# Kernel tuning notes

Measured on AMD Instinct MI355X. Metric: run time of the kernel, lower is better.

The kernel has to match this reference:

```python
import jax, jax.numpy as jnp
import numpy as np

B, T, D, H = 512, 200, 128, 128


def setup_inputs() -> dict:
    key = jax.random.key(0)
    ks = jax.random.split(key, 16)
    r = lambda k, shp, s=0.05: jax.random.normal(k, shp, dtype=jnp.float32) * s
    F = 3 * D + H  # concat([item_eb, his_sum, item_eb*his_sum, final_state2])
    return {
        "item_eb": jax.random.normal(ks[0], (B, D), dtype=jnp.float32),
        "item_his_eb": jax.random.normal(ks[1], (B, T, D), dtype=jnp.float32),
        "Wg1": r(ks[2], (D + H, 2 * H)), "bg1": jnp.ones((2 * H,), jnp.float32),
        "Wc1": r(ks[3], (D + H, H)), "bc1": jnp.zeros((H,), jnp.float32),
        "att_w1": r(ks[4], (4 * H, 80)), "att_b1": jnp.zeros((80,), jnp.float32),
        "att_w2": r(ks[5], (80, 40)), "att_b2": jnp.zeros((40,), jnp.float32),
        "att_w3": r(ks[6], (40, 1)), "att_b3": jnp.zeros((1,), jnp.float32),
        "Wg2": r(ks[7], (2 * H, 2 * H)), "bg2": jnp.ones((2 * H,), jnp.float32),
        "Wc2": r(ks[8], (2 * H, H)), "bc2": jnp.zeros((H,), jnp.float32),
        "fc1_w": r(ks[9], (F, 200)), "fc1_b": jnp.zeros((200,), jnp.float32),
        "alpha1": jnp.full((200,), 0.25, jnp.float32),
        "fc2_w": r(ks[10], (200, 80)), "fc2_b": jnp.zeros((80,), jnp.float32),
        "alpha2": jnp.full((80,), 0.25, jnp.float32),
        "fc3_w": r(ks[11], (80, 2)), "fc3_b": jnp.zeros((2,), jnp.float32),
        "seq_len": jax.random.randint(ks[12], (B,), 1, T + 1).astype(jnp.int32),
    }


def _gru_scan(x_btd, Wg, bg, Wc, bc, seq_len, att=None):
    """GRU (TF GRUCell math) or AUGRU if att [B,T] is given.
    Honors sequence_length semantics of tf dynamic_rnn: state copied through,
    outputs zeroed past each row's length."""
    Bx, Tx, _ = x_btd.shape
    Hh = Wc.shape[1]
    xs = jnp.swapaxes(x_btd, 0, 1)  # [T,B,Din]
    ts = jnp.arange(Tx)
    a_ts = jnp.swapaxes(att, 0, 1) if att is not None else jnp.zeros((Tx, Bx), x_btd.dtype)
    h0 = jnp.zeros((Bx, Hh), x_btd.dtype)

    def step(h, xat):
        x, a, t = xat
        gates = jax.nn.sigmoid(jnp.concatenate([x, h], axis=-1) @ Wg + bg)
        rg, u = jnp.split(gates, 2, axis=-1)
        c = jnp.tanh(jnp.concatenate([x, rg * h], axis=-1) @ Wc + bc)
        if att is not None:  # VecAttGRUCell: u = (1 - att_score) * u
            u = (1.0 - a[:, None]) * u
        hn = u * h + (1.0 - u) * c
        valid = (t < seq_len)[:, None]
        hn = jnp.where(valid, hn, h)
        out = jnp.where(valid, hn, jnp.zeros_like(hn))
        return hn, out

    hT, outs = jax.lax.scan(step, h0, (xs, a_ts, ts))
    return jnp.swapaxes(outs, 0, 1), hT  # [B,T,H], [B,H]


def _forward(item_eb, item_his_eb, Wg1, bg1, Wc1, bc1, att_w1, att_b1, att_w2, att_b2,
             att_w3, att_b3, Wg2, bg2, Wc2, bc2, fc1_w, fc1_b, alpha1, fc2_w, fc2_b,
             alpha2, fc3_w, fc3_b, seq_len):
    Bx, Tx, Dx = item_his_eb.shape
    mask = jnp.arange(Tx)[None, :] < seq_len[:, None]  # [B,T] bool
    # rnn_1: plain GRU over history embeddings
    rnn1, _ = _gru_scan(item_his_eb, Wg1, bg1, Wc1, bc1, seq_len)
    # din_fcn_attention: concat trick + 3-layer scorer + masked softmax
    q = jnp.broadcast_to(item_eb[:, None, :], rnn1.shape)
    din_all = jnp.concatenate([q, rnn1, q - rnn1, q * rnn1], axis=-1)  # [B,T,4H]
    h1 = jax.nn.sigmoid(din_all @ att_w1 + att_b1)
    h2 = jax.nn.sigmoid(h1 @ att_w2 + att_b2)
    scores = (h2 @ att_w3 + att_b3)[..., 0]  # [B,T]
    NEG_INF = jnp.float32(-(2.0 ** 32) + 1.0)  # DIEN padding value
    scores = jnp.where(mask, scores, NEG_INF)
    alphas = jax.nn.softmax(scores, axis=-1)  # [B,T]
    # rnn_2: AUGRU (VecAttGRUCell) gated by attention scores; take final state
    _, final_state2 = _gru_scan(rnn1, Wg2, bg2, Wc2, bc2, seq_len, att=alphas)
    # fcn head on concatenated features
    his_sum = jnp.sum(item_his_eb * mask[..., None].astype(item_his_eb.dtype), axis=1)
    feat = jnp.concatenate([item_eb, his_sum, item_eb * his_sum, final_state2], axis=-1)
    prelu = lambda x, a: jnp.maximum(x, 0.0) + a * jnp.minimum(x, 0.0)
    z = prelu(feat @ fc1_w + fc1_b, alpha1)
    z = prelu(z @ fc2_w + fc2_b, alpha2)
    logits = z @ fc3_w + fc3_b  # [B,2]
    return jax.nn.softmax(logits, axis=-1)


def reference(item_eb, item_his_eb, Wg1, bg1, Wc1, bc1, att_w1, att_b1, att_w2, att_b2,
              att_w3, att_b3, Wg2, bg2, Wc2, bc2, fc1_w, fc1_b, alpha1, fc2_w, fc2_b,
              alpha2, fc3_w, fc3_b, seq_len):
    return _forward(item_eb, item_his_eb, Wg1, bg1, Wc1, bc1, att_w1, att_b1, att_w2,
                    att_b2, att_w3, att_b3, Wg2, bg2, Wc2, bc2, fc1_w, fc1_b, alpha1,
                    fc2_w, fc2_b, alpha2, fc3_w, fc3_b, seq_len)
```

## Files before the change

### kernel.cpp

```cpp
#include <hip/hip_runtime.h>
#include <hip/hip_bf16.h>


typedef __attribute__((ext_vector_type(8))) short bf16x8;
typedef __attribute__((ext_vector_type(4))) float f32x4;
typedef _Float16 f16x2 __attribute__((ext_vector_type(2)));

#define NC 4
#define TC 50
#define CROWS 25600
#define CSH 3276800

static __device__ __forceinline__ unsigned short f2bf(float f) {
  union { __hip_bfloat16 h; unsigned short u; } v;
  v.h = __float2bfloat16(f);
  return v.u;
}
static __device__ __forceinline__ float bf2f(unsigned short u) {
  union { __hip_bfloat16 h; unsigned short u; } v;
  v.u = u;
  return __bfloat162float(v.h);
}
static __device__ __forceinline__ unsigned short f2h(float f) {
  union { _Float16 h; unsigned short u; } v;
  v.h = (_Float16)f;
  return v.u;
}
static __device__ __forceinline__ float h2f(unsigned short u) {
  union { unsigned short u; _Float16 h; } v;
  v.u = u;
  return (float)v.h;
}
static __device__ __forceinline__ unsigned int pkf16(float a, float b) {
  union { f16x2 v; unsigned int u; } c;
  c.v = (f16x2){(_Float16)a, (_Float16)b};
  return c.u;
}
static __device__ __forceinline__ void dot2a(float& acc, unsigned int w, unsigned int h) {
  asm volatile("v_dot2_f32_f16 %0, %1, %2, %0" : "+v"(acc) : "v"(w), "v"(h));
}
static __device__ __forceinline__ void gbar() {
  __builtin_amdgcn_sched_barrier(0);
  asm volatile("s_waitcnt lgkmcnt(0)" ::: "memory");
  __builtin_amdgcn_s_barrier();
  __builtin_amdgcn_sched_barrier(0);
}

__global__ __launch_bounds__(256) void prep_weights(
    const float* __restrict__ item_eb,
    const float* __restrict__ Wg1, const float* __restrict__ Wc1,
    const float* __restrict__ Wg2, const float* __restrict__ Wc2,
    const float* __restrict__ aw1, const float* __restrict__ aw2,
    const float* __restrict__ aw3,
    const float* __restrict__ bg1, const float* __restrict__ bc1,
    const float* __restrict__ bg2, const float* __restrict__ bc2,
    const float* __restrict__ ab1, const float* __restrict__ ab2,
    unsigned short* __restrict__ W1xT, unsigned short* __restrict__ W2xT,
    unsigned short* __restrict__ AW1T, unsigned short* __restrict__ AW2T,
    float* __restrict__ b384_1, float* __restrict__ b384_2,
    float* __restrict__ bA1, float* __restrict__ bA2,
    unsigned int* __restrict__ WgP1, unsigned int* __restrict__ WcP1,
    unsigned int* __restrict__ WgP2, unsigned int* __restrict__ WcP2,
    float* __restrict__ w3p, unsigned short* __restrict__ Xq,
    float* __restrict__ hstate)
{
  int e = blockIdx.x * 256 + threadIdx.x;
  if (e < 49152) {
    int n = e >> 7, k = e & 127;
    float v1 = (n < 256) ? Wg1[k * 256 + n] : Wc1[k * 128 + (n - 256)];
    float v2 = (n < 256) ? Wg2[k * 256 + n] : Wc2[k * 128 + (n - 256)];
    W1xT[e] = f2bf(v1);
    W2xT[e] = f2bf(v2);
  }
  if (e < 65536) {
    int n = e >> 9, k = e & 511;
    AW1T[e] = f2bf(n < 80 ? aw1[k * 80 + n] : 0.f);
    Xq[e] = f2bf(item_eb[e]);
    hstate[e] = 0.f;
  }
  if (e < 16384) {
    int n = e >> 7, k = e & 127;
    AW2T[e] = f2bf((n < 40 && k < 80) ? aw2[k * 40 + n] : 0.f);
  }
  if (e < 16384) {
    int i = e >> 8, tt = e & 255;
    int row = 128 + 2 * i;
    WgP1[e] = pkf16(Wg1[row * 256 + tt], Wg1[(row + 1) * 256 + tt]);
    WgP2[e] = pkf16(Wg2[row * 256 + tt], Wg2[(row + 1) * 256 + tt]);
  }
  if (e < 8192) {
    int i = e >> 8, tt = e & 255;
    int jc = tt >> 1, half = tt & 1;
    int row = 128 + half * 64 + 2 * i;
    WcP1[e] = pkf16(Wc1[row * 128 + jc], Wc1[(row + 1) * 128 + jc]);
    WcP2[e] = pkf16(Wc2[row * 128 + jc], Wc2[(row + 1) * 128 + jc]);
  }
  if (e < 384) {
    b384_1[e] = (e < 256) ? bg1[e] : bc1[e - 256];
    b384_2[e] = (e < 256) ? bg2[e] : bc2[e - 256];
  }
  if (e < 128) {
    bA1[e] = (e < 80) ? ab1[e] : 0.f;
    bA2[e] = (e < 40) ? ab2[e] : 0.f;
    w3p[e] = (e < 40) ? aw3[e] : 0.f;
  }
}

__global__ __launch_bounds__(256) void cast_his_t(const float4* __restrict__ in4,
                                                  ushort4* __restrict__ out4)
{
  int i = blockIdx.x * 256 + threadIdx.x;
  float4 v = in4[i];
  int d4 = (i & 31) << 2;
  int bt = i >> 5;
  int tt = bt % 200, bb = bt / 200;
  out4[(((size_t)tt * 512 + bb) * 128 + d4) >> 2] =
      make_ushort4(f2bf(v.x), f2bf(v.y), f2bf(v.z), f2bf(v.w));
}

struct GemmP {
  const unsigned short* A;
  const unsigned short* B;
  const float* bias;
  unsigned short* out;
  float* scores;
  const float* w3p;
  const float* b3;
  const unsigned short* Xq;
  const unsigned short* rnn1;
  long rowbase;
  int K, ldc, mtiles, tbase;
};

static __device__ __forceinline__ uint4 bfop(uint4 q, uint4 r, bool mul) {
  unsigned short* qs = (unsigned short*)&q;
  unsigned short* rs = (unsigned short*)&r;
  uint4 o;
  unsigned short* os = (unsigned short*)&o;
#pragma unroll
  for (int i = 0; i < 8; i++) {
    float a = bf2f(qs[i]), b = bf2f(rs[i]);
    os[i] = f2bf(mul ? a * b : a - b);
  }
  return o;
}

template <int SRC, int EPI>
__device__ __forceinline__ void gemm_body(const GemmP& P, int tile, char* smem) {
  uint4* AsB = (uint4*)smem;
  uint4* BsB = AsB + 1024;
  const int tid = threadIdx.x;
  const int w = tid >> 6, l = tid & 63;
  const int mb = tile % P.mtiles, nb = tile / P.mtiles;
  const long mBase = (long)mb * 128;
  const int nBase = nb * 128;

  f32x4 acc[2][8];
#pragma unroll
  for (int m = 0; m < 2; m++)
#pragma unroll
    for (int n = 0; n < 8; n++) acc[m][n] = 0.f;

  const int srow = (tid >> 3) & 31;
  const int scc = l & 7;
  const int KK = SRC ? 512 : P.K;

  for (int kb = 0; kb < KK; kb += 64) {
#pragma unroll
    for (int p = 0; p < 4; p++) {
      int row = p * 32 + srow;
      long grow = mBase + row;
      uint4 va;
      if (SRC == 0) {
        va = *(const uint4*)(P.A + (size_t)grow * KK + kb + scc * 8);
      } else {
        int seg = kb >> 7;
        int c0 = (kb & 127) + scc * 8;
        int b = (int)(grow & 511);
        if (seg == 0) {
          va = *(const uint4*)(P.Xq + b * 128 + c0);
        } else if (seg == 1) {
          va = *(const uint4*)(P.rnn1 + (size_t)(P.rowbase + grow) * 128 + c0);
        } else {
          uint4 vq = *(const uint4*)(P.Xq + b * 128 + c0);
          uint4 vr = *(const uint4*)(P.rnn1 + (size_t)(P.rowbase + grow) * 128 + c0);
          va = bfop(vq, vr, seg == 3);
        }
      }
      uint4 vb = *(const uint4*)(P.B + (size_t)(nBase + row) * KK + kb + scc * 8);
      AsB[row * 8 + (scc ^ (row & 7))] = va;
      BsB[row * 8 + (scc ^ (row & 7))] = vb;
    }
    __syncthreads();
#pragma unroll
    for (int ks = 0; ks < 2; ks++) {
      int ccr = ks * 4 + (l >> 4);
      int r0 = w * 32 + (l & 15);
      int r1 = r0 + 16;
      bf16x8 a0 = *(const bf16x8*)&AsB[r0 * 8 + (ccr ^ (r0 & 7))];
      bf16x8 a1 = *(const bf16x8*)&AsB[r1 * 8 + (ccr ^ (r1 & 7))];
#pragma unroll
      for (int n = 0; n < 8; n++) {
        int rb = n * 16 + (l & 15);
        bf16x8 bn = *(const bf16x8*)&BsB[rb * 8 + (ccr ^ (rb & 7))];
        acc[0][n] = __builtin_amdgcn_mfma_f32_16x16x32_bf16(a0, bn, acc[0][n], 0, 0, 0);
        acc[1][n] = __builtin_amdgcn_mfma_f32_16x16x32_bf16(a1, bn, acc[1][n], 0, 0, 0);
      }
    }
    __syncthreads();
  }

  const int lcol = l & 15, lrow4 = (l >> 4) * 4;
  if (EPI == 2) {
    float sp[2][4] = {{0.f, 0.f, 0.f, 0.f}, {0.f, 0.f, 0.f, 0.f}};
#pragma unroll
    for (int n = 0; n < 8; n++) {
      int gcol = n * 16 + lcol;
      float bb = P.bias[gcol];
      float w3 = P.w3p[gcol];
#pragma unroll
      for (int m = 0; m < 2; m++)
#pragma unroll
        for (int i = 0; i < 4; i++) {
          float v = acc[m][n][i] + bb;
          sp[m][i] += w3 / (1.f + __expf(-v));
        }
    }
#pragma unroll
    for (int msk = 1; msk < 16; msk <<= 1)
#pragma unroll
      for (int m = 0; m < 2; m++)
#pragma unroll
        for (int i = 0; i < 4; i++) sp[m][i] += __shfl_xor(sp[m][i], msk);
    float b3v = P.b3[0];
    if (lcol == 0) {
#pragma unroll
      for (int m = 0; m < 2; m++)
#pragma unroll
        for (int i = 0; i < 4; i++) {
          long grow = mBase + w * 32 + m * 16 + lrow4 + i;
          int b = (int)(grow & 511);
          int tp = (int)(grow >> 9) + P.tbase;
          P.scores[b * 200 + tp] = sp[m][i] + b3v;
        }
    }
  } else {
#pragma unroll
    for (int n = 0; n < 8; n++) {
      int gcol = nBase + n * 16 + lcol;
      float bb = P.bias[gcol];
#pragma unroll
      for (int m = 0; m < 2; m++)
#pragma unroll
        for (int i = 0; i < 4; i++) {
          long grow = mBase + w * 32 + m * 16 + lrow4 + i;
          float v = acc[m][n][i] + bb;
          if (EPI == 0) P.out[grow * P.ldc + gcol] = f2h(v);
          else          P.out[grow * P.ldc + gcol] = f2bf(1.f / (1.f + __expf(-v)));
        }
    }
  }
}

struct GruP {
  const unsigned short* xproj;
  const unsigned int* WgP;
  const unsigned int* WcP;
  const int* seqlen;
  const float* alphas;
  unsigned short* outbf;
  float* hstate;
  int tbase;
};

template <int AUGRU>
__device__ void gru_body(const GruP& P, int r, char* smem) {
  float* hF = (float*)smem;
  float* uF = hF + 128;
  unsigned int* hH = (unsigned int*)(uF + 128);
  unsigned int* rghP = hH + 64;
  const int t = threadIdx.x;
  const int jc = t >> 1;
  const int len = P.seqlen[r];
  int nsteps = len - P.tbase;
  if (nsteps > TC) nsteps = TC;

  if (nsteps <= 0) {
    if (!AUGRU && t < 64) {
      for (int s = 0; s < TC; s++)
        ((unsigned int*)(P.outbf + ((size_t)(P.tbase + s) * 512 + r) * 128))[t] = 0;
    }
    return;
  }
  __builtin_amdgcn_s_setprio(1);

  unsigned int wg[64], wc[32];
#pragma unroll
  for (int i = 0; i < 64; i++) wg[i] = P.WgP[i * 256 + t];
#pragma unroll
  for (int i = 0; i < 32; i++) wc[i] = P.WcP[i * 256 + t];

  if (t < 128) hF[t] = P.hstate[r * 128 + t];
  if (t < 64) hH[t] = pkf16(P.hstate[r * 128 + 2 * t], P.hstate[r * 128 + 2 * t + 1]);
  gbar();

  const unsigned short* xp = P.xproj;
  const size_t RS = (size_t)512 * 384;
  const size_t base = (size_t)r * 384;
  unsigned short gA = xp[base + t], cA = xp[base + 256 + jc];
  int s1 = nsteps > 1 ? 1 : 0;
  unsigned short gB = xp[s1 * RS + base + t], cB = xp[s1 * RS + base + 256 + jc];
  float alA = AUGRU ? P.alphas[r * 200 + P.tbase] : 0.f;
  float alB = AUGRU ? P.alphas[r * 200 + P.tbase + s1] : 0.f;

  for (int ts = 0; ts < nsteps; ++ts) {
    int tsn = (ts + 2 < nsteps) ? ts + 2 : nsteps - 1;
    size_t off = (size_t)tsn * RS + base;
    unsigned short gC = xp[off + t];
    unsigned short cC = xp[off + 256 + jc];
    float alC = AUGRU ? P.alphas[r * 200 + P.tbase + tsn] : 0.f;

    float a0 = 0.f, a1 = 0.f, a2 = 0.f, a3 = 0.f;
#pragma unroll
    for (int q = 0; q < 4; q++) {
      uint4 h0 = *(const uint4*)&hH[q * 16 + 0];
      uint4 h1 = *(const uint4*)&hH[q * 16 + 4];
      uint4 h2 = *(const uint4*)&hH[q * 16 + 8];
      uint4 h3 = *(const uint4*)&hH[q * 16 + 12];
      dot2a(a0, wg[q * 16 + 0], h0.x);  dot2a(a1, wg[q * 16 + 1], h0.y);
      dot2a(a2, wg[q * 16 + 2], h0.z);  dot2a(a3, wg[q * 16 + 3], h0.w);
      dot2a(a0, wg[q * 16 + 4], h1.x);  dot2a(a1, wg[q * 16 + 5], h1.y);
      dot2a(a2, wg[q * 16 + 6], h1.z);  dot2a(a3, wg[q * 16 + 7], h1.w);
      dot2a(a0, wg[q * 16 + 8], h2.x);  dot2a(a1, wg[q * 16 + 9], h2.y);
      dot2a(a2, wg[q * 16 + 10], h2.z); dot2a(a3, wg[q * 16 + 11], h2.w);
      dot2a(a0, wg[q * 16 + 12], h3.x); dot2a(a1, wg[q * 16 + 13], h3.y);
      dot2a(a2, wg[q * 16 + 14], h3.z); dot2a(a3, wg[q * 16 + 15], h3.w);
    }
    float a = (a0 + a1) + (a2 + a3) + h2f(gA);
    float g = 1.f / (1.f + __expf(-a));
    if (t < 128) {
      float rgh = g * hF[t];
      float rh2 = __shfl_down(rgh, 1);
      if (!(t & 1)) rghP[t >> 1] = pkf16(rgh, rh2);
    } else {
      uF[t - 128] = g;
    }
    gbar();

    float c0 = 0.f, c1 = 0.f;
    const uint4* rp = (const uint4*)&rghP[(t & 1) * 32];
#pragma unroll
    for (int q = 0; q < 8; q++) {
      uint4 rq = rp[q];
      dot2a(c0, wc[q * 4 + 0], rq.x);
      dot2a(c1, wc[q * 4 + 1], rq.y);
      dot2a(c0, wc[q * 4 + 2], rq.z);
      dot2a(c1, wc[q * 4 + 3], rq.w);
    }
    float c = c0 + c1;
    c += __shfl_xor(c, 1);
    c += h2f(cA);
    c = fminf(fmaxf(c, -15.f), 15.f);
    float e2 = __expf(2.f * c);
    c = 1.f - 2.f / (e2 + 1.f);
    float u = uF[jc];
    if (AUGRU) u *= (1.f - alA);
    float h = hF[jc];
    float hn = u * h + (1.f - u) * c;
    float hnHi = __shfl_down(hn, 2);
    if (!(t & 1)) {
      hF[jc] = hn;
      if (!AUGRU) P.outbf[((size_t)(P.tbase + ts) * 512 + r) * 128 + jc] = f2bf(hn);
    }
    if (!(t & 3)) hH[t >> 2] = pkf16(hn, hnHi);
    gbar();

    gA = gB; cA = cB; alA = alB;
    gB = gC; cB = cC; alB = alC;
  }

  if (t < 128) P.hstate[r * 128 + t] = hF[t];
  if (!AUGRU && nsteps < TC && t < 64) {
    for (int s = nsteps; s < TC; s++)
      ((unsigned int*)(P.outbf + ((size_t)(P.tbase + s) * 512 + r) * 128))[t] = 0;
  }
}

__device__ void hsum_body(const float* __restrict__ his, float* __restrict__ hs,
                          const int* __restrict__ seqlen, int b, char* smem) {
  float* sm = (float*)smem;
  int t = threadIdx.x;
  int len = seqlen[b];
  int col = t & 127, hf = t >> 7;
  float s = 0.f;
  for (int ts = hf; ts < len; ts += 2) s += his[((size_t)b * 200 + ts) * 128 + col];
  sm[t] = s;
  __syncthreads();
  if (t < 128) hs[b * 128 + t] = sm[t] + sm[t + 128];
}

template <int AUG, int GRU, int S1, int E1, int S2, int E2, int S3, int E3, int HS>
__global__ __launch_bounds__(256) void fatk(GruP gp, GemmP p1, int c1,
                                            GemmP p2, int c2, GemmP p3,
                                            const float* hisp, float* hsp)
{
  extern __shared__ char smem[];
  int id = blockIdx.x;
  if constexpr (GRU) {
    if (id < 512) { gru_body<AUG>(gp, id, smem); return; }
    id -= 512;
  }
  if constexpr (HS) {
    if (id < 512) { hsum_body(hisp, hsp, gp.seqlen, id, smem); return; }
    id -= 512;
  }
  if constexpr (S1 >= 0) {
    if (id < c1) { gemm_body<S1, E1>(p1, id, smem); return; }
    id -= c1;
  }
  if constexpr (S2 >= 0) {
    if (id < c2) { gemm_body<S2, E2>(p2, id, smem); return; }
    id -= c2;
  }
  if constexpr (S3 >= 0) gemm_body<S3, E3>(p3, id, smem);
}

__global__ __launch_bounds__(256) void mask_softmax(
    const float* __restrict__ scores, const int* __restrict__ seqlen,
    float* __restrict__ alphas, float* __restrict__ hstate)
{
  int b = blockIdx.x, t = threadIdx.x;
  __shared__ float red[256];
  if (t < 128) hstate[b * 128 + t] = 0.f;
  int len = seqlen[b];
  float s = (t < 200 && t < len) ? scores[b * 200 + t] : -1e30f;
  red[t] = s;
  __syncthreads();
  for (int o = 128; o > 0; o >>= 1) {
    if (t < o) red[t] = fmaxf(red[t], red[t + o]);
    __syncthreads();
  }
  float m = red[0];
  __syncthreads();
  float e = (t < 200 && t < len) ? __expf(s - m) : 0.f;
  red[t] = e;
  __syncthreads();
  for (int o = 128; o > 0; o >>= 1) {
    if (t < o) red[t] += red[t + o];
    __syncthreads();
  }
  float denom = red[0];
  if (t < 200) alphas[b * 200 + t] = e / denom;
}

__global__ __launch_bounds__(256) void head_kernel(
    const float* __restrict__ item_eb, const float* __restrict__ hs,
    const float* __restrict__ hstate,
    const float* __restrict__ w1, const float* __restrict__ b1, const float* __restrict__ a1,
    const float* __restrict__ w2, const float* __restrict__ b2, const float* __restrict__ a2,
    const float* __restrict__ w3, const float* __restrict__ b3,
    float* __restrict__ out)
{
  int b = blockIdx.x, t = threadIdx.x;
  __shared__ float frow[512];
  __shared__ float z1[200];
  __shared__ float z2[80];
  if (t < 128) {
    float sv = hs[b * 128 + t];
    float q = item_eb[b * 128 + t];
    frow[t] = q;
    frow[128 + t] = sv;
    frow[256 + t] = q * sv;
    frow[384 + t] = hstate[b * 128 + t];
  }
  __syncthreads();
  if (t < 200) {
    float acc = b1[t];
#pragma unroll 8
    for (int k = 0; k < 512; k++) acc += frow[k] * w1[k * 200 + t];
    z1[t] = acc > 0.f ? acc : a1[t] * acc;
  }
  __syncthreads();
  if (t < 80) {
    float acc = b2[t];
#pragma unroll 8
    for (int k = 0; k < 200; k++) acc += z1[k] * w2[k * 80 + t];
    z2[t] = acc > 0.f ? acc : a2[t] * acc;
  }
  __syncthreads();
  if (t == 0) {
    float l0 = b3[0], l1 = b3[1];
    for (int k = 0; k < 80; k++) {
      float z = z2[k];
      l0 += z * w3[k * 2];
      l1 += z * w3[k * 2 + 1];
    }
    float m = fmaxf(l0, l1);
    float e0 = __expf(l0 - m), e1 = __expf(l1 - m);
    out[b * 2 + 0] = e0 / (e0 + e1);
    out[b * 2 + 1] = e1 / (e0 + e1);
  }
}

extern "C" void kernel_launch(void* const* d_in, const int* in_sizes, int n_in,
                              void* d_out, int out_size, void* d_ws, size_t ws_size,
                              hipStream_t stream)
{
  const float* item_eb = (const float*)d_in[0];
  const float* his     = (const float*)d_in[1];
  const float* Wg1     = (const float*)d_in[2];
  const float* bg1     = (const float*)d_in[3];
  const float* Wc1     = (const float*)d_in[4];
  const float* bc1     = (const float*)d_in[5];
  const float* aw1     = (const float*)d_in[6];
  const float* ab1     = (const float*)d_in[7];
  const float* aw2     = (const float*)d_in[8];
  const float* ab2     = (const float*)d_in[9];
  const float* aw3     = (const float*)d_in[10];
  const float* ab3     = (const float*)d_in[11];
  const float* Wg2     = (const float*)d_in[12];
  const float* bg2     = (const float*)d_in[13];
  const float* Wc2     = (const float*)d_in[14];
  const float* bc2     = (const float*)d_in[15];
  const float* fc1w    = (const float*)d_in[16];
  const float* fc1b    = (const float*)d_in[17];
  const float* al1     = (const float*)d_in[18];
  const float* fc2w    = (const float*)d_in[19];
  const float* fc2b    = (const float*)d_in[20];
  const float* al2     = (const float*)d_in[21];
  const float* fc3w    = (const float*)d_in[22];
  const float* fc3b    = (const float*)d_in[23];
  const int*   seqlen  = (const int*)d_in[24];

  char* ws = (char*)d_ws;
  unsigned short* XhA    = (unsigned short*)(ws + 0L);
  unsigned short* xpA    = (unsigned short*)(ws + 26214400L);
  unsigned short* xpB    = (unsigned short*)(ws + 45875200L);
  unsigned short* rnn1   = (unsigned short*)(ws + 65536000L);
  float*          scores = (float*)(ws + 91750400L);
  float*          alphas = (float*)(ws + 92160000L);
  float*          hstate = (float*)(ws + 92569600L);
  unsigned int*   WgP1   = (unsigned int*)(ws + 92831744L);
  unsigned int*   WcP1   = (unsigned int*)(ws + 92897280L);
  unsigned int*   WgP2   = (unsigned int*)(ws + 92930048L);
  unsigned int*   WcP2   = (unsigned int*)(ws + 92995584L);
  unsigned short* W1xT   = (unsigned short*)(ws + 93028352L);
  unsigned short* W2xT   = (unsigned short*)(ws + 93126656L);
  unsigned short* AW1T   = (unsigned short*)(ws + 93224960L);
  unsigned short* AW2T   = (unsigned short*)(ws + 93356032L);
  float*          b384_1 = (float*)(ws + 93388800L);
  float*          b384_2 = (float*)(ws + 93390336L);
  float*          bA1    = (float*)(ws + 93391872L);
  float*          bA2    = (float*)(ws + 93392384L);
  float*          w3p    = (float*)(ws + 93392896L);
  unsigned short* Xq     = (unsigned short*)(ws + 93393408L);
  float*          hs     = scores;

  unsigned short* h1[NC] = {XhA, XhA + CSH, XhA + 2 * CSH, XhA + 3 * CSH};

  const int SM = 32768;
  GruP gz{}; GemmP dz{};
  gz.seqlen = seqlen;

  auto mkGru = [&](int c, int aug) {
    GruP g;
    g.xproj = (c & 1) ? xpB : xpA;
    g.WgP = aug ? WgP2 : WgP1; g.WcP = aug ? WcP2 : WcP1;
    g.seqlen = seqlen; g.alphas = alphas;
    g.outbf = aug ? nullptr : rnn1; g.hstate = hstate; g.tbase = c * TC;
    return g;
  };
  auto mkXp = [&](const unsigned short* A, const float* bias, unsigned short* outp) {
    GemmP p{}; p.A = A; p.B = (bias == b384_1) ? W1xT : W2xT; p.bias = bias;
    p.out = outp; p.K = 128; p.ldc = 384; p.mtiles = 200; return p;
  };
  auto mkAtt1 = [&](int c) {
    GemmP p{}; p.B = AW1T; p.bias = bA1; p.out = h1[c];
    p.Xq = Xq; p.rnn1 = rnn1; p.rowbase = (long)c * CROWS;
    p.K = 512; p.ldc = 128; p.mtiles = 200; return p;
  };
  auto mkAtt2 = [&](int c) {
    GemmP p{}; p.A = h1[c]; p.B = AW2T; p.bias = bA2;
    p.scores = scores; p.w3p = w3p; p.b3 = ab3;
    p.K = 128; p.ldc = 128; p.mtiles = 200; p.tbase = c * TC; return p;
  };

  prep_weights<<<256, 256, 0, stream>>>(item_eb, Wg1, Wc1, Wg2, Wc2, aw1, aw2, aw3,
                                        bg1, bc1, bg2, bc2, ab1, ab2,
                                        W1xT, W2xT, AW1T, AW2T, b384_1, b384_2, bA1, bA2,
                                        WgP1, WcP1, WgP2, WcP2, w3p, Xq, hstate);
  cast_his_t<<<12800, 256, 0, stream>>>((const float4*)his, (ushort4*)XhA);

  fatk<0,0, 0,0, -1,0, -1,0, 0><<<600, 256, SM, stream>>>(
      gz, mkXp(XhA, b384_1, xpA), 600, dz, 0, dz, nullptr, nullptr);
  fatk<0,1, 0,0, -1,0, -1,0, 0><<<1112, 256, SM, stream>>>(
      mkGru(0,0), mkXp(XhA + (size_t)CSH, b384_1, xpB), 600, dz, 0, dz, nullptr, nullptr);
  fatk<0,1, 0,0, -1,0, -1,0, 0><<<1112, 256, SM, stream>>>(
      mkGru(1,0), mkXp(XhA + (size_t)2*CSH, b384_1, xpA), 600, dz, 0, dz, nullptr, nullptr);
  fatk<0,1, 0,0, 1,1, -1,0, 0><<<1712, 256, SM, stream>>>(
      mkGru(2,0), mkXp(XhA + (size_t)3*CSH, b384_1, xpB), 600, mkAtt1(0), 200, dz, nullptr, nullptr);
  fatk<0,1, 1,1, 0,2, -1,0, 0><<<912, 256, SM, stream>>>(
      mkGru(3,0), mkAtt1(1), 200, mkAtt2(0), 200, dz, nullptr, nullptr);
  fatk<0,0, 1,1, 0,2, 0,0, 0><<<1000, 256, SM, stream>>>(
      gz, mkAtt1(2), 200, mkAtt2(1), 200, mkXp(rnn1, b384_2, xpA), nullptr, nullptr);
  fatk<0,0, 1,1, 0,2, 0,0, 0><<<1000, 256, SM, stream>>>(
      gz, mkAtt1(3), 200, mkAtt2(2), 200, mkXp(rnn1 + (size_t)CSH, b384_2, xpB), nullptr, nullptr);
  fatk<0,0, 0,2, -1,0, -1,0, 0><<<200, 256, SM, stream>>>(
      gz, mkAtt2(3), 200, dz, 0, dz, nullptr, nullptr);
  mask_softmax<<<512, 256, 0, stream>>>(scores, seqlen, alphas, hstate);
  fatk<1,1, -1,0, -1,0, -1,0, 1><<<1024, 256, SM, stream>>>(
      mkGru(0,1), dz, 0, dz, 0, dz, his, hs);
  fatk<1,1, 0,0, -1,0, -1,0, 0><<<1112, 256, SM, stream>>>(
      mkGru(1,1), mkXp(rnn1 + (size_t)2*CSH, b384_2, xpA), 600, dz, 0, dz, nullptr, nullptr);
  fatk<1,1, 0,0, -1,0, -1,0, 0><<<1112, 256, SM, stream>>>(
      mkGru(2,1), mkXp(rnn1 + (size_t)3*CSH, b384_2, xpB), 600, dz, 0, dz, nullptr, nullptr);
  fatk<1,1, -1,0, -1,0, -1,0, 0><<<512, 256, SM, stream>>>(
      mkGru(3,1), dz, 0, dz, 0, dz, nullptr, nullptr);
  head_kernel<<<512, 256, 0, stream>>>(item_eb, hs, hstate,
                                       fc1w, fc1b, al1, fc2w, fc2b, al2,
                                       fc3w, fc3b, (float*)d_out);
}
```

Before: 664.2 us.

## Pack two GRU rows per block with one thread per hidden unit

Restructures the recurrent GRU body so each 256-thread block processes two batch rows, with 128 threads per row and each thread owning one hidden unit. Each thread holds its reset, update and candidate weight columns in registers (192 registers of packed f16 pairs), which removes the cross-lane shuffles, the split gate layout and the extra shared-memory u/h buffers. The GRU block count drops from 512 to 256. The trade-offs are much higher register pressure, which may cause spills or lower occupancy, and the two rows in a block now run for the longer row's step count, with per-step validity masking for the shorter one.

```diff
diff --git a/kernel.cpp b/kernel.cpp
--- a/kernel.cpp
+++ b/kernel.cpp
@@ -59,8 +59,10 @@
     unsigned short* __restrict__ AW1T, unsigned short* __restrict__ AW2T,
     float* __restrict__ b384_1, float* __restrict__ b384_2,
     float* __restrict__ bA1, float* __restrict__ bA2,
-    unsigned int* __restrict__ WgP1, unsigned int* __restrict__ WcP1,
-    unsigned int* __restrict__ WgP2, unsigned int* __restrict__ WcP2,
+    unsigned int* __restrict__ WgrP1, unsigned int* __restrict__ WguP1,
+    unsigned int* __restrict__ WcP1,
+    unsigned int* __restrict__ WgrP2, unsigned int* __restrict__ WguP2,
+    unsigned int* __restrict__ WcP2,
     float* __restrict__ w3p, unsigned short* __restrict__ Xq,
     float* __restrict__ hstate)
 {
@@ -82,18 +84,15 @@
     int n = e >> 7, k = e & 127;
     AW2T[e] = f2bf((n < 40 && k < 80) ? aw2[k * 40 + n] : 0.f);
   }
-  if (e < 16384) {
-    int i = e >> 8, tt = e & 255;
+  if (e < 8192) {
+    int i = e >> 7, tt = e & 127;
     int row = 128 + 2 * i;
-    WgP1[e] = pkf16(Wg1[row * 256 + tt], Wg1[(row + 1) * 256 + tt]);
-    WgP2[e] = pkf16(Wg2[row * 256 + tt], Wg2[(row + 1) * 256 + tt]);
-  }
-  if (e < 8192) {
-    int i = e >> 8, tt = e & 255;
-    int jc = tt >> 1, half = tt & 1;
-    int row = 128 + half * 64 + 2 * i;
-    WcP1[e] = pkf16(Wc1[row * 128 + jc], Wc1[(row + 1) * 128 + jc]);
-    WcP2[e] = pkf16(Wc2[row * 128 + jc], Wc2[(row + 1) * 128 + jc]);
+    WgrP1[e] = pkf16(Wg1[row * 256 + tt],       Wg1[(row + 1) * 256 + tt]);
+    WguP1[e] = pkf16(Wg1[row * 256 + 128 + tt], Wg1[(row + 1) * 256 + 128 + tt]);
+    WcP1[e]  = pkf16(Wc1[row * 128 + tt],       Wc1[(row + 1) * 128 + tt]);
+    WgrP2[e] = pkf16(Wg2[row * 256 + tt],       Wg2[(row + 1) * 256 + tt]);
+    WguP2[e] = pkf16(Wg2[row * 256 + 128 + tt], Wg2[(row + 1) * 256 + 128 + tt]);
+    WcP2[e]  = pkf16(Wc2[row * 128 + tt],       Wc2[(row + 1) * 128 + tt]);
   }
   if (e < 384) {
     b384_1[e] = (e < 256) ? bg1[e] : bc1[e - 256];
@@ -264,8 +263,9 @@
 
 struct GruP {
   const unsigned short* xproj;
-  const unsigned int* WgP;
-  const unsigned int* WcP;
+  const unsigned int* Wgr;
+  const unsigned int* Wgu;
+  const unsigned int* Wc;
   const int* seqlen;
   const float* alphas;
   unsigned short* outbf;
@@ -274,115 +274,140 @@
 };
 
 template <int AUGRU>
-__device__ void gru_body(const GruP& P, int r, char* smem) {
-  float* hF = (float*)smem;
-  float* uF = hF + 128;
-  unsigned int* hH = (unsigned int*)(uF + 128);
-  unsigned int* rghP = hH + 64;
+__device__ void gru_body(const GruP& P, int rblk, char* smem) {
   const int t = threadIdx.x;
-  const int jc = t >> 1;
-  const int len = P.seqlen[r];
-  int nsteps = len - P.tbase;
-  if (nsteps > TC) nsteps = TC;
-
-  if (nsteps <= 0) {
-    if (!AUGRU && t < 64) {
+  const int team = t >> 7, tt = t & 127;
+  const int r = rblk * 2 + team;
+  const int lenA = P.seqlen[rblk * 2], lenB = P.seqlen[rblk * 2 + 1];
+  const int len = team ? lenB : lenA;
+  int nsA = lenA - P.tbase; if (nsA > TC) nsA = TC;
+  int nsB = lenB - P.tbase; if (nsB > TC) nsB = TC;
+  int bsteps = nsA > nsB ? nsA : nsB;
+
+  if (bsteps <= 0) {
+    if (!AUGRU) {
       for (int s = 0; s < TC; s++)
-        ((unsigned int*)(P.outbf + ((size_t)(P.tbase + s) * 512 + r) * 128))[t] = 0;
+        P.outbf[((size_t)(P.tbase + s) * 512 + r) * 128 + tt] = 0;
     }
     return;
   }
   __builtin_amdgcn_s_setprio(1);
 
-  unsigned int wg[64], wc[32];
-#pragma unroll
-  for (int i = 0; i < 64; i++) wg[i] = P.WgP[i * 256 + t];
-#pragma unroll
-  for (int i = 0; i < 32; i++) wc[i] = P.WcP[i * 256 + t];
-
-  if (t < 128) hF[t] = P.hstate[r * 128 + t];
-  if (t < 64) hH[t] = pkf16(P.hstate[r * 128 + 2 * t], P.hstate[r * 128 + 2 * t + 1]);
+  unsigned int wgr[64], wgu[64], wcv[64];
+#pragma unroll
+  for (int i = 0; i < 64; i++) wgr[i] = P.Wgr[i * 128 + tt];
+#pragma unroll
+  for (int i = 0; i < 64; i++) wgu[i] = P.Wgu[i * 128 + tt];
+#pragma unroll
+  for (int i = 0; i < 64; i++) wcv[i] = P.Wc[i * 128 + tt];
+
+  unsigned short* hHh  = (unsigned short*)smem + team * 256;
+  unsigned short* rghH = hHh + 128;
+
+  float h = P.hstate[r * 128 + tt];
+  hHh[tt] = f2h(h);
   gbar();
 
   const unsigned short* xp = P.xproj;
   const size_t RS = (size_t)512 * 384;
   const size_t base = (size_t)r * 384;
-  unsigned short gA = xp[base + t], cA = xp[base + 256 + jc];
-  int s1 = nsteps > 1 ? 1 : 0;
-  unsigned short gB = xp[s1 * RS + base + t], cB = xp[s1 * RS + base + 256 + jc];
-  float alA = AUGRU ? P.alphas[r * 200 + P.tbase] : 0.f;
-  float alB = AUGRU ? P.alphas[r * 200 + P.tbase + s1] : 0.f;
-
-  for (int ts = 0; ts < nsteps; ++ts) {
-    int tsn = (ts + 2 < nsteps) ? ts + 2 : nsteps - 1;
+  unsigned short gR0 = xp[base + tt];
+  unsigned short gU0 = xp[base + 128 + tt];
+  unsigned short cX0 = xp[base + 256 + tt];
+  int s1 = bsteps > 1 ? 1 : 0;
+  unsigned short gR1 = xp[s1 * RS + base + tt];
+  unsigned short gU1 = xp[s1 * RS + base + 128 + tt];
+  unsigned short cX1 = xp[s1 * RS + base + 256 + tt];
+  float al0 = AUGRU ? P.alphas[r * 200 + P.tbase] : 0.f;
+  float al1 = AUGRU ? P.alphas[r * 200 + P.tbase + s1] : 0.f;
+
+  for (int ts = 0; ts < bsteps; ++ts) {
+    int tsn = (ts + 2 < bsteps) ? ts + 2 : bsteps - 1;
     size_t off = (size_t)tsn * RS + base;
-    unsigned short gC = xp[off + t];
-    unsigned short cC = xp[off + 256 + jc];
-    float alC = AUGRU ? P.alphas[r * 200 + P.tbase + tsn] : 0.f;
-
-    float a0 = 0.f, a1 = 0.f, a2 = 0.f, a3 = 0.f;
+    unsigned short gRn = xp[off + tt];
+    unsigned short gUn = xp[off + 128 + tt];
+    unsigned short cXn = xp[off + 256 + tt];
+    float aln = AUGRU ? P.alphas[r * 200 + P.tbase + tsn] : 0.f;
+
+    float ar0 = 0.f, ar1 = 0.f, ar2 = 0.f, ar3 = 0.f;
+    float au0 = 0.f, au1 = 0.f, au2 = 0.f, au3 = 0.f;
+    const uint4* hw = (const uint4*)hHh;
 #pragma unroll
     for (int q = 0; q < 4; q++) {
-      uint4 h0 = *(const uint4*)&hH[q * 16 + 0];
-      uint4 h1 = *(const uint4*)&hH[q * 16 + 4];
-      uint4 h2 = *(const uint4*)&hH[q * 16 + 8];
-      uint4 h3 = *(const uint4*)&hH[q * 16 + 12];
-      dot2a(a0, wg[q * 16 + 0], h0.x);  dot2a(a1, wg[q * 16 + 1], h0.y);
-      dot2a(a2, wg[q * 16 + 2], h0.z);  dot2a(a3, wg[q * 16 + 3], h0.w);
-      dot2a(a0, wg[q * 16 + 4], h1.x);  dot2a(a1, wg[q * 16 + 5], h1.y);
-      dot2a(a2, wg[q * 16 + 6], h1.z);  dot2a(a3, wg[q * 16 + 7], h1.w);
-      dot2a(a0, wg[q * 16 + 8], h2.x);  dot2a(a1, wg[q * 16 + 9], h2.y);
-      dot2a(a2, wg[q * 16 + 10], h2.z); dot2a(a3, wg[q * 16 + 11], h2.w);
-      dot2a(a0, wg[q * 16 + 12], h3.x); dot2a(a1, wg[q * 16 + 13], h3.y);
-      dot2a(a2, wg[q * 16 + 14], h3.z); dot2a(a3, wg[q * 16 + 15], h3.w);
-    }
-    float a = (a0 + a1) + (a2 + a3) + h2f(gA);
-    float g = 1.f / (1.f + __expf(-a));
-    if (t < 128) {
-      float rgh = g * hF[t];
-      float rh2 = __shfl_down(rgh, 1);
-      if (!(t & 1)) rghP[t >> 1] = pkf16(rgh, rh2);
-    } else {
-      uF[t - 128] = g;
-    }
+      uint4 h0 = hw[q * 4 + 0];
+      uint4 h1 = hw[q * 4 + 1];
+      uint4 h2 = hw[q * 4 + 2];
+      uint4 h3 = hw[q * 4 + 3];
+      dot2a(ar0, wgr[q * 16 + 0], h0.x);  dot2a(au0, wgu[q * 16 + 0], h0.x);
+      dot2a(ar1, wgr[q * 16 + 1], h0.y);  dot2a(au1, wgu[q * 16 + 1], h0.y);
+      dot2a(ar2, wgr[q * 16 + 2], h0.z);  dot2a(au2, wgu[q * 16 + 2], h0.z);
+      dot2a(ar3, wgr[q * 16 + 3], h0.w);  dot2a(au3, wgu[q * 16 + 3], h0.w);
+      dot2a(ar0, wgr[q * 16 + 4], h1.x);  dot2a(au0, wgu[q * 16 + 4], h1.x);
+      dot2a(ar1, wgr[q * 16 + 5], h1.y);  dot2a(au1, wgu[q * 16 + 5], h1.y);
+      dot2a(ar2, wgr[q * 16 + 6], h1.z);  dot2a(au2, wgu[q * 16 + 6], h1.z);
+      dot2a(ar3, wgr[q * 16 + 7], h1.w);  dot2a(au3, wgu[q * 16 + 7], h1.w);
+      dot2a(ar0, wgr[q * 16 + 8], h2.x);  dot2a(au0, wgu[q * 16 + 8], h2.x);
+      dot2a(ar1, wgr[q * 16 + 9], h2.y);  dot2a(au1, wgu[q * 16 + 9], h2.y);
+      dot2a(ar2, wgr[q * 16 + 10], h2.z); dot2a(au2, wgu[q * 16 + 10], h2.z);
+      dot2a(ar3, wgr[q * 16 + 11], h2.w); dot2a(au3, wgu[q * 16 + 11], h2.w);
+      dot2a(ar0, wgr[q * 16 + 12], h3.x); dot2a(au0, wgu[q * 16 + 12], h3.x);
+      dot2a(ar1, wgr[q * 16 + 13], h3.y); dot2a(au1, wgu[q * 16 + 13], h3.y);
+      dot2a(ar2, wgr[q * 16 + 14], h3.z); dot2a(au2, wgu[q * 16 + 14], h3.z);
+      dot2a(ar3, wgr[q * 16 + 15], h3.w); dot2a(au3, wgu[q * 16 + 15], h3.w);
+    }
+    float ar = (ar0 + ar1) + (ar2 + ar3) + h2f(gR0);
+    float au = (au0 + au1) + (au2 + au3) + h2f(gU0);
+    float rg = 1.f / (1.f + __expf(-ar));
+    float u  = 1.f / (1.f + __expf(-au));
+    rghH[tt] = f2h(rg * h);
     gbar();
 
-    float c0 = 0.f, c1 = 0.f;
-    const uint4* rp = (const uint4*)&rghP[(t & 1) * 32];
-#pragma unroll
-    for (int q = 0; q < 8; q++) {
-      uint4 rq = rp[q];
-      dot2a(c0, wc[q * 4 + 0], rq.x);
-      dot2a(c1, wc[q * 4 + 1], rq.y);
-      dot2a(c0, wc[q * 4 + 2], rq.z);
-      dot2a(c1, wc[q * 4 + 3], rq.w);
-    }
-    float c = c0 + c1;
-    c += __shfl_xor(c, 1);
-    c += h2f(cA);
+    float c0 = 0.f, c1 = 0.f, c2 = 0.f, c3 = 0.f;
+    const uint4* rw = (const uint4*)rghH;
+#pragma unroll
+    for (int q = 0; q < 4; q++) {
+      uint4 r0 = rw[q * 4 + 0];
+      uint4 r1 = rw[q * 4 + 1];
+      uint4 r2 = rw[q * 4 + 2];
+      uint4 r3 = rw[q * 4 + 3];
+      dot2a(c0, wcv[q * 16 + 0], r0.x);
+      dot2a(c1, wcv[q * 16 + 1], r0.y);
+      dot2a(c2, wcv[q * 16 + 2], r0.z);
+      dot2a(c3, wcv[q * 16 + 3], r0.w);
+      dot2a(c0, wcv[q * 16 + 4], r1.x);
+      dot2a(c1, wcv[q * 16 + 5], r1.y);
+      dot2a(c2, wcv[q * 16 + 6], r1.z);
+      dot2a(c3, wcv[q * 16 + 7], r1.w);
+      dot2a(c0, wcv[q * 16 + 8], r2.x);
+      dot2a(c1, wcv[q * 16 + 9], r2.y);
+      dot2a(c2, wcv[q * 16 + 10], r2.z);
+      dot2a(c3, wcv[q * 16 + 11], r2.w);
+      dot2a(c0, wcv[q * 16 + 12], r3.x);
+      dot2a(c1, wcv[q * 16 + 13], r3.y);
+      dot2a(c2, wcv[q * 16 + 14], r3.z);
+      dot2a(c3, wcv[q * 16 + 15], r3.w);
+    }
+    float c = (c0 + c1) + (c2 + c3) + h2f(cX0);
     c = fminf(fmaxf(c, -15.f), 15.f);
     float e2 = __expf(2.f * c);
     c = 1.f - 2.f / (e2 + 1.f);
-    float u = uF[jc];
-    if (AUGRU) u *= (1.f - alA);
-    float h = hF[jc];
-    float hn = u * h + (1.f - u) * c;
-    float hnHi = __shfl_down(hn, 2);
-    if (!(t & 1)) {
-      hF[jc] = hn;
-      if (!AUGRU) P.outbf[((size_t)(P.tbase + ts) * 512 + r) * 128 + jc] = f2bf(hn);
-    }
-    if (!(t & 3)) hH[t >> 2] = pkf16(hn, hnHi);
+    float ue = AUGRU ? u * (1.f - al0) : u;
+    float hn = ue * h + (1.f - ue) * c;
+    bool valid = (P.tbase + ts) < len;
+    h = valid ? hn : h;
+    hHh[tt] = f2h(h);
+    if (!AUGRU)
+      P.outbf[((size_t)(P.tbase + ts) * 512 + r) * 128 + tt] = valid ? f2bf(h) : 0;
     gbar();
 
-    gA = gB; cA = cB; alA = alB;
-    gB = gC; cB = cC; alB = alC;
-  }
-
-  if (t < 128) P.hstate[r * 128 + t] = hF[t];
-  if (!AUGRU && nsteps < TC && t < 64) {
-    for (int s = nsteps; s < TC; s++)
-      ((unsigned int*)(P.outbf + ((size_t)(P.tbase + s) * 512 + r) * 128))[t] = 0;
+    gR0 = gR1; gU0 = gU1; cX0 = cX1; al0 = al1;
+    gR1 = gRn; gU1 = gUn; cX1 = cXn; al1 = aln;
+  }
+
+  P.hstate[r * 128 + tt] = h;
+  if (!AUGRU) {
+    for (int s = bsteps; s < TC; s++)
+      P.outbf[((size_t)(P.tbase + s) * 512 + r) * 128 + tt] = 0;
   }
 }
 
@@ -407,8 +432,8 @@
   extern __shared__ char smem[];
   int id = blockIdx.x;
   if constexpr (GRU) {
-    if (id < 512) { gru_body<AUG>(gp, id, smem); return; }
-    id -= 512;
+    if (id < 256) { gru_body<AUG>(gp, id, smem); return; }
+    id -= 256;
   }
   if constexpr (HS) {
     if (id < 512) { hsum_body(hisp, hsp, gp.seqlen, id, smem); return; }
@@ -540,9 +565,11 @@
   float*          scores = (float*)(ws + 91750400L);
   float*          alphas = (float*)(ws + 92160000L);
   float*          hstate = (float*)(ws + 92569600L);
-  unsigned int*   WgP1   = (unsigned int*)(ws + 92831744L);
+  unsigned int*   WgrP1  = (unsigned int*)(ws + 92831744L);
+  unsigned int*   WguP1  = (unsigned int*)(ws + 92864512L);
   unsigned int*   WcP1   = (unsigned int*)(ws + 92897280L);
-  unsigned int*   WgP2   = (unsigned int*)(ws + 92930048L);
+  unsigned int*   WgrP2  = (unsigned int*)(ws + 92930048L);
+  unsigned int*   WguP2  = (unsigned int*)(ws + 92962816L);
   unsigned int*   WcP2   = (unsigned int*)(ws + 92995584L);
   unsigned short* W1xT   = (unsigned short*)(ws + 93028352L);
   unsigned short* W2xT   = (unsigned short*)(ws + 93126656L);
@@ -565,7 +592,9 @@
   auto mkGru = [&](int c, int aug) {
     GruP g;
     g.xproj = (c & 1) ? xpB : xpA;
-    g.WgP = aug ? WgP2 : WgP1; g.WcP = aug ? WcP2 : WcP1;
+    g.Wgr = aug ? WgrP2 : WgrP1;
+    g.Wgu = aug ? WguP2 : WguP1;
+    g.Wc  = aug ? WcP2  : WcP1;
     g.seqlen = seqlen; g.alphas = alphas;
     g.outbf = aug ? nullptr : rnn1; g.hstate = hstate; g.tbase = c * TC;
     return g;
@@ -588,18 +617,19 @@
   prep_weights<<<256, 256, 0, stream>>>(item_eb, Wg1, Wc1, Wg2, Wc2, aw1, aw2, aw3,
                                         bg1, bc1, bg2, bc2, ab1, ab2,
                                         W1xT, W2xT, AW1T, AW2T, b384_1, b384_2, bA1, bA2,
-                                        WgP1, WcP1, WgP2, WcP2, w3p, Xq, hstate);
+                                        WgrP1, WguP1, WcP1, WgrP2, WguP2, WcP2,
+                                        w3p, Xq, hstate);
   cast_his_t<<<12800, 256, 0, stream>>>((const float4*)his, (ushort4*)XhA);
 
   fatk<0,0, 0,0, -1,0, -1,0, 0><<<600, 256, SM, stream>>>(
       gz, mkXp(XhA, b384_1, xpA), 600, dz, 0, dz, nullptr, nullptr);
-  fatk<0,1, 0,0, -1,0, -1,0, 0><<<1112, 256, SM, stream>>>(
+  fatk<0,1, 0,0, -1,0, -1,0, 0><<<856, 256, SM, stream>>>(
       mkGru(0,0), mkXp(XhA + (size_t)CSH, b384_1, xpB), 600, dz, 0, dz, nullptr, nullptr);
-  fatk<0,1, 0,0, -1,0, -1,0, 0><<<1112, 256, SM, stream>>>(
+  fatk<0,1, 0,0, -1,0, -1,0, 0><<<856, 256, SM, stream>>>(
       mkGru(1,0), mkXp(XhA + (size_t)2*CSH, b384_1, xpA), 600, dz, 0, dz, nullptr, nullptr);
-  fatk<0,1, 0,0, 1,1, -1,0, 0><<<1712, 256, SM, stream>>>(
+  fatk<0,1, 0,0, 1,1, -1,0, 0><<<1056, 256, SM, stream>>>(
       mkGru(2,0), mkXp(XhA + (size_t)3*CSH, b384_1, xpB), 600, mkAtt1(0), 200, dz, nullptr, nullptr);
-  fatk<0,1, 1,1, 0,2, -1,0, 0><<<912, 256, SM, stream>>>(
+  fatk<0,1, 1,1, 0,2, -1,0, 0><<<656, 256, SM, stream>>>(
       mkGru(3,0), mkAtt1(1), 200, mkAtt2(0), 200, dz, nullptr, nullptr);
   fatk<0,0, 1,1, 0,2, 0,0, 0><<<1000, 256, SM, stream>>>(
       gz, mkAtt1(2), 200, mkAtt2(1), 200, mkXp(rnn1, b384_2, xpA), nullptr, nullptr);
@@ -608,13 +638,13 @@
   fatk<0,0, 0,2, -1,0, -1,0, 0><<<200, 256, SM, stream>>>(
       gz, mkAtt2(3), 200, dz, 0, dz, nullptr, nullptr);
   mask_softmax<<<512, 256, 0, stream>>>(scores, seqlen, alphas, hstate);
-  fatk<1,1, -1,0, -1,0, -1,0, 1><<<1024, 256, SM, stream>>>(
+  fatk<1,1, -1,0, -1,0, -1,0, 1><<<768, 256, SM, stream>>>(
       mkGru(0,1), dz, 0, dz, 0, dz, his, hs);
-  fatk<1,1, 0,0, -1,0, -1,0, 0><<<1112, 256, SM, stream>>>(
+  fatk<1,1, 0,0, -1,0, -1,0, 0><<<856, 256, SM, stream>>>(
       mkGru(1,1), mkXp(rnn1 + (size_t)2*CSH, b384_2, xpA), 600, dz, 0, dz, nullptr, nullptr);
-  fatk<1,1, 0,0, -1,0, -1,0, 0><<<1112, 256, SM, stream>>>(
+  fatk<1,1, 0,0, -1,0, -1,0, 0><<<856, 256, SM, stream>>>(
       mkGru(2,1), mkXp(rnn1 + (size_t)3*CSH, b384_2, xpB), 600, dz, 0, dz, nullptr, nullptr);
-  fatk<1,1, -1,0, -1,0, -1,0, 0><<<512, 256, SM, stream>>>(
+  fatk<1,1, -1,0, -1,0, -1,0, 0><<<256, 256, SM, stream>>>(
       mkGru(3,1), dz, 0, dz, 0, dz, nullptr, nullptr);
   head_kernel<<<512, 256, 0, stream>>>(item_eb, hs, hstate,
                                        fc1w, fc1b, al1, fc2w, fc2b, al2,
```

After: 715.4 us. 7.7% more time.
